# Kernel optimization log

Hardware: AMD Instinct MI355X
Metric: run time of the kernel (lower is better)

The kernel has to match this reference:

```python
import jax, jax.numpy as jnp
import numpy as np

B, D, H, O, E = 8192, 1024, 4096, 1024, 3

def setup_inputs() -> dict:
    key = jax.random.key(0)
    ks = jax.random.split(key, 8)
    s = lambda fan_in: 1.0 / np.sqrt(fan_in)
    return {
        "x":   jax.random.normal(ks[0], (B, D), jnp.float32),
        "gw1": jax.random.normal(ks[1], (D, 256), jnp.float32) * s(D),
        "gb1": jnp.zeros((256,), jnp.float32),
        "gw2": jax.random.normal(ks[2], (256, 128), jnp.float32) * s(256),
        "gb2": jnp.zeros((128,), jnp.float32),
        "gw3": jax.random.normal(ks[3], (128, E), jnp.float32) * s(128),
        "gb3": jnp.zeros((E,), jnp.float32),
        "ew1": jax.random.normal(ks[4], (E, D, H), jnp.float32) * s(D),
        "eb1": jnp.zeros((E, H), jnp.float32),
        "ew2": jax.random.normal(ks[5], (E, H, O), jnp.float32) * s(H),
        "eb2": jnp.zeros((E, O), jnp.float32),
        "top_k": 2,
    }

def reference(x, gw1, gb1, gw2, gb2, gw3, gb3, ew1, eb1, ew2, eb2, top_k):
    # Gating network (dropout is identity in eval mode)
    g = jax.nn.relu(x @ gw1 + gb1)
    g = jax.nn.relu(g @ gw2 + gb2)
    gates = jax.nn.softmax(g @ gw3 + gb3, axis=-1)          # [B, E]

    # top-k routing with renormalized weights
    topk_scores, topk_idx = jax.lax.top_k(gates, top_k)     # [B, k]
    topk_scores = topk_scores / jnp.sum(topk_scores, axis=-1, keepdims=True)

    # scatter normalized scores into dense [B, E] combine weights
    b_ix = jnp.arange(x.shape[0])[:, None]
    combine = jnp.zeros_like(gates).at[b_ix, topk_idx].add(topk_scores)  # [B, E]

    # run all experts densely (small E=3), combine with routing weights
    eh = jax.nn.relu(jnp.einsum('bd,edh->beh', x, ew1) + eb1[None])      # [B, E, H]
    eo = jnp.einsum('beh,eho->beo', eh, ew2) + eb2[None]                 # [B, E, O]
    out = jnp.einsum('be,beo->bo', combine, eo)                          # [B, O]
    return out, gates
```

## Files before the change

### kernel.cpp

```cpp
#include <hip/hip_runtime.h>
#include <cstdint>
#include <cstddef>

#define B_ROWS 8192
#define D_DIM  1024
#define H_DIM  4096
#define O_DIM  1024
#define E_NUM  3
#define K2     (2 * H_DIM)
#define MT_MAX 66
#define SLOT_MAX (MT_MAX * 128)

typedef __attribute__((ext_vector_type(4))) float f4;
typedef __attribute__((ext_vector_type(8))) _Float16 half8;

__device__ __forceinline__ unsigned short f2h_bits(float f) {
  _Float16 h = (_Float16)f;
  return __builtin_bit_cast(unsigned short, h);
}

__device__ __forceinline__ void async16(const void* g, void* l) {
  __builtin_amdgcn_global_load_lds(
      (const __attribute__((address_space(1))) unsigned int*)g,
      (__attribute__((address_space(3))) unsigned int*)l, 16, 0, 0);
}

__global__ __launch_bounds__(256) void k_cast_x(const float* __restrict__ in,
                                                unsigned short* __restrict__ out) {
  size_t i = (size_t)blockIdx.x * 256 + threadIdx.x;
  const f4* p = (const f4*)in;
  f4 a = p[2 * i], b = p[2 * i + 1];
  half8 h;
#pragma unroll
  for (int j = 0; j < 4; ++j) { h[j] = (_Float16)a[j]; h[4 + j] = (_Float16)b[j]; }
  *(half8*)(out + 8 * i) = h;
}

__global__ __launch_bounds__(256) void k_transpose_cast(const float* __restrict__ in,
                                                        unsigned short* __restrict__ out,
                                                        int R, int C) {
  __shared__ float tile[32][33];
  const size_t eoff = (size_t)blockIdx.z * R * C;
  const float* I = in + eoff;
  unsigned short* O = out + eoff;
  int c0 = blockIdx.x * 32, r0 = blockIdx.y * 32;
  int tx = threadIdx.x & 31, ty = threadIdx.x >> 5;
#pragma unroll
  for (int i = 0; i < 4; ++i)
    tile[ty + 8 * i][tx] = I[(size_t)(r0 + ty + 8 * i) * C + c0 + tx];
  __syncthreads();
#pragma unroll
  for (int i = 0; i < 4; ++i)
    O[(size_t)(c0 + ty + 8 * i) * R + r0 + tx] = f2h_bits(tile[tx][ty + 8 * i]);
}

__global__ __launch_bounds__(256) void k_gemm_f32(const float* __restrict__ A,
                                                  const float* __restrict__ Bm,
                                                  const float* __restrict__ bias,
                                                  float* __restrict__ C,
                                                  int N, int K) {
  __shared__ float sAT[16][68];
  __shared__ float sB[16][68];
  const int t = threadIdx.x;
  const int tx = t & 15, ty = t >> 4;
  const int m0 = blockIdx.y * 64, n0 = blockIdx.x * 64;
  float acc[4][4] = {};
  for (int k0 = 0; k0 < K; k0 += 16) {
    __syncthreads();
#pragma unroll
    for (int i = 0; i < 4; ++i) {
      int idx = t + i * 256;
      int r = idx >> 4, c = idx & 15;
      sAT[c][r] = A[(size_t)(m0 + r) * K + (k0 + c)];
      int rb = idx >> 6, cb = idx & 63;
      sB[rb][cb] = Bm[(size_t)(k0 + rb) * N + (n0 + cb)];
    }
    __syncthreads();
#pragma unroll
    for (int kk = 0; kk < 16; ++kk) {
      f4 av = *(const f4*)&sAT[kk][ty * 4];
      f4 bv = *(const f4*)&sB[kk][tx * 4];
#pragma unroll
      for (int i = 0; i < 4; ++i)
#pragma unroll
        for (int j = 0; j < 4; ++j)
          acc[i][j] = fmaf(av[i], bv[j], acc[i][j]);
    }
  }
#pragma unroll
  for (int i = 0; i < 4; ++i) {
    int row = m0 + ty * 4 + i;
    f4 v;
#pragma unroll
    for (int j = 0; j < 4; ++j)
      v[j] = fmaxf(acc[i][j] + bias[n0 + tx * 4 + j], 0.f);
    *(f4*)&C[(size_t)row * N + n0 + tx * 4] = v;
  }
}

__global__ __launch_bounds__(256) void k_gate_topk(const float* __restrict__ h2,
                                                   const float* __restrict__ gw3,
                                                   const float* __restrict__ gb3,
                                                   float* __restrict__ gates,
                                                   float* __restrict__ combine,
                                                   int* __restrict__ bucket) {
  const int lane = threadIdx.x & 63;
  const int row = blockIdx.x * 4 + (threadIdx.x >> 6);
  const float* h = h2 + (size_t)row * 128;
  float h0 = h[lane], h1 = h[lane + 64];
  float l0 = h0 * gw3[lane * 3 + 0] + h1 * gw3[(lane + 64) * 3 + 0];
  float l1 = h0 * gw3[lane * 3 + 1] + h1 * gw3[(lane + 64) * 3 + 1];
  float l2 = h0 * gw3[lane * 3 + 2] + h1 * gw3[(lane + 64) * 3 + 2];
#pragma unroll
  for (int off = 32; off > 0; off >>= 1) {
    l0 += __shfl_down(l0, off);
    l1 += __shfl_down(l1, off);
    l2 += __shfl_down(l2, off);
  }
  if (lane == 0) {
    float g0 = l0 + gb3[0], g1v = l1 + gb3[1], g2v = l2 + gb3[2];
    float mx = fmaxf(g0, fmaxf(g1v, g2v));
    float e0 = expf(g0 - mx), e1 = expf(g1v - mx), e2 = expf(g2v - mx);
    float inv = 1.f / (e0 + e1 + e2);
    float p0 = e0 * inv, p1 = e1 * inv, p2 = e2 * inv;
    gates[row * 3 + 0] = p0; gates[row * 3 + 1] = p1; gates[row * 3 + 2] = p2;
    int amin = 0; float pm = p0;
    if (p1 <= pm) { pm = p1; amin = 1; }
    if (p2 <= pm) { pm = p2; amin = 2; }
    float denom = (p0 + p1 + p2) - pm;
    combine[row * 3 + 0] = (amin == 0) ? 0.f : p0 / denom;
    combine[row * 3 + 1] = (amin == 1) ? 0.f : p1 / denom;
    combine[row * 3 + 2] = (amin == 2) ? 0.f : p2 / denom;
    bucket[row] = amin;
  }
}

__global__ __launch_bounds__(256) void k_count(const int* __restrict__ bucket,
                                               int* __restrict__ cnt) {
  int row = blockIdx.x * 256 + threadIdx.x;
  int b = bucket[row];
  int lane = threadIdx.x & 63;
#pragma unroll
  for (int bid = 0; bid < 3; ++bid) {
    unsigned long long m = __ballot(b == bid);
    if (m && b == bid) {
      int prefix = __popcll(m & ((1ull << lane) - 1));
      if (prefix == 0) atomicAdd(&cnt[bid], __popcll(m));
    }
  }
}

__global__ void k_meta(const int* __restrict__ cnt, int* __restrict__ meta,
                       int* __restrict__ cnt2) {
  int t0 = (cnt[0] + 127) >> 7;
  int t1 = (cnt[1] + 127) >> 7;
  int t2 = (cnt[2] + 127) >> 7;
  meta[0] = 0; meta[1] = t0; meta[2] = t0 + t1; meta[3] = t0 + t1 + t2;
  cnt2[0] = 0; cnt2[1] = 0; cnt2[2] = 0;
}

__global__ __launch_bounds__(256) void k_scatter(const int* __restrict__ bucket,
                                                 const int* __restrict__ meta,
                                                 int* __restrict__ cnt2,
                                                 int* __restrict__ sorted) {
  int row = blockIdx.x * 256 + threadIdx.x;
  int b = bucket[row];
  int lane = threadIdx.x & 63;
#pragma unroll
  for (int bid = 0; bid < 3; ++bid) {
    unsigned long long m = __ballot(b == bid);
    if (m) {
      int cntm = __popcll(m);
      int leader = __ffsll((unsigned long long)m) - 1;
      int base = 0;
      if (lane == leader) base = atomicAdd(&cnt2[bid], cntm);
      base = __shfl(base, leader);
      if (b == bid) {
        int prefix = __popcll(m & ((1ull << lane) - 1));
        sorted[meta[bid] * 128 + base + prefix] = row;
      }
    }
  }
}

__device__ __forceinline__ void bucket_experts(int b, int& ea, int& eb) {
  ea = (b == 0) ? 1 : 0;
  eb = (b == 2) ? 1 : 2;
}

__global__ __launch_bounds__(256) void k_expert_h(const unsigned short* __restrict__ Xh,
                                                  const unsigned short* __restrict__ W1T,
                                                  const float* __restrict__ combine,
                                                  const float* __restrict__ eb1,
                                                  const int* __restrict__ sorted,
                                                  const int* __restrict__ meta,
                                                  unsigned short* __restrict__ EHS) {
  constexpr int K = D_DIM;
  const int mt = blockIdx.x;
  const int tb1 = meta[1], tb2 = meta[2], tb3 = meta[3];
  if (mt >= tb3) return;
  const int b = (mt >= tb2) ? 2 : (mt >= tb1) ? 1 : 0;
  int ea, ebx; bucket_experts(b, ea, ebx);
  const int z = blockIdx.z;
  const int e = z ? ebx : ea;
  const int slot0 = ((b == 0) ? 0 : (b == 1) ? tb1 : tb2) * 128 + (mt - ((b == 0) ? 0 : (b == 1) ? tb1 : tb2)) * 128;
  const int n0 = blockIdx.y * 128;

  __shared__ __align__(16) char smem[32768];
  __shared__ float sC[128];
  char* sA = smem;
  char* sB = smem + 16384;
  const int t = threadIdx.x;
  if (t < 128) {
    int r = sorted[slot0 + t];
    sC[t] = (r < 0) ? 0.f : combine[(size_t)r * 3 + e];
  }

  const unsigned short* aptr[4];
  const unsigned short* bptr[4];
  int soff[4];
#pragma unroll
  for (int i = 0; i < 4; ++i) {
    int sa = t + i * 256;
    int row = sa >> 3;
    int j = (sa & 7) ^ (row & 7);
    soff[i] = sa * 16;
    int r = sorted[slot0 + row];
    int rr = (r < 0) ? 0 : r;
    aptr[i] = Xh + (size_t)rr * K + j * 8;
    bptr[i] = W1T + (size_t)e * H_DIM * K + (size_t)(n0 + row) * K + j * 8;
  }
  const int lane = t & 63;
  const int wm = (t >> 6) & 1, wn = t >> 7;
  const int quad = lane >> 4, l16 = lane & 15;
  int offA[4][2], offB[4][2];
#pragma unroll
  for (int mtile = 0; mtile < 4; ++mtile) {
    int ra = wm * 64 + mtile * 16 + l16;
    int rb = wn * 64 + mtile * 16 + l16;
#pragma unroll
    for (int s = 0; s < 2; ++s) {
      offA[mtile][s] = ra * 128 + (((s * 4 + quad) ^ (ra & 7)) * 16);
      offB[mtile][s] = rb * 128 + (((s * 4 + quad) ^ (rb & 7)) * 16);
    }
  }
  f4 acc[4][4] = {};
  for (int k0 = 0; k0 < K; k0 += 64) {
#pragma unroll
    for (int i = 0; i < 4; ++i) {
      async16(aptr[i] + k0, sA + soff[i]);
      async16(bptr[i] + k0, sB + soff[i]);
    }
    __syncthreads();
#pragma unroll
    for (int s = 0; s < 2; ++s) {
      half8 a[4], bfr[4];
#pragma unroll
      for (int i = 0; i < 4; ++i) a[i] = *(const half8*)(sA + offA[i][s]);
#pragma unroll
      for (int i = 0; i < 4; ++i) bfr[i] = *(const half8*)(sB + offB[i][s]);
#pragma unroll
      for (int i = 0; i < 4; ++i)
#pragma unroll
        for (int jn = 0; jn < 4; ++jn)
          acc[i][jn] = __builtin_amdgcn_mfma_f32_16x16x32_f16(a[i], bfr[jn], acc[i][jn], 0, 0, 0);
    }
    __syncthreads();
  }
  const float* bias = eb1 + (size_t)e * H_DIM;
#pragma unroll
  for (int nt = 0; nt < 4; ++nt) {
    int col = n0 + wn * 64 + nt * 16 + l16;
    float bb = bias[col];
#pragma unroll
    for (int mtile = 0; mtile < 4; ++mtile) {
#pragma unroll
      for (int r = 0; r < 4; ++r) {
        int rloc = wm * 64 + mtile * 16 + quad * 4 + r;
        float v = fmaxf(acc[mtile][nt][r] + bb, 0.f) * sC[rloc];
        EHS[(size_t)(slot0 + rloc) * K2 + (size_t)z * H_DIM + col] = f2h_bits(v);
      }
    }
  }
}

__global__ __launch_bounds__(256) void k_expert_o(const unsigned short* __restrict__ EHS,
                                                  const unsigned short* __restrict__ W2T,
                                                  const float* __restrict__ combine,
                                                  const float* __restrict__ eb2,
                                                  const int* __restrict__ sorted,
                                                  const int* __restrict__ meta,
                                                  float* __restrict__ OUT) {
  const int mt = blockIdx.x;
  const int tb1 = meta[1], tb2 = meta[2], tb3 = meta[3];
  if (mt >= tb3) return;
  const int b = (mt >= tb2) ? 2 : (mt >= tb1) ? 1 : 0;
  int ea, ebx; bucket_experts(b, ea, ebx);
  const int slot0 = mt * 128;
  const int n0 = blockIdx.y * 128;

  __shared__ __align__(16) char smem[32768];
  __shared__ int sRow[128];
  __shared__ float sCa[128], sCb[128];
  char* sA = smem;
  char* sB = smem + 16384;
  const int t = threadIdx.x;
  if (t < 128) {
    int r = sorted[slot0 + t];
    sRow[t] = r;
    int rr = (r < 0) ? 0 : r;
    sCa[t] = combine[(size_t)rr * 3 + ea];
    sCb[t] = combine[(size_t)rr * 3 + ebx];
  }

  const unsigned short* ap[4];
  size_t bpo[4];
  int soff[4];
#pragma unroll
  for (int i = 0; i < 4; ++i) {
    int sa = t + i * 256;
    int row = sa >> 3;
    int j = (sa & 7) ^ (row & 7);
    soff[i] = sa * 16;
    ap[i] = EHS + (size_t)(slot0 + row) * K2 + j * 8;
    bpo[i] = (size_t)(n0 + row) * H_DIM + j * 8;
  }
  const int lane = t & 63;
  const int wm = (t >> 6) & 1, wn = t >> 7;
  const int quad = lane >> 4, l16 = lane & 15;
  int offA[4][2], offB[4][2];
#pragma unroll
  for (int mtile = 0; mtile < 4; ++mtile) {
    int ra = wm * 64 + mtile * 16 + l16;
    int rb = wn * 64 + mtile * 16 + l16;
#pragma unroll
    for (int s = 0; s < 2; ++s) {
      offA[mtile][s] = ra * 128 + (((s * 4 + quad) ^ (ra & 7)) * 16);
      offB[mtile][s] = rb * 128 + (((s * 4 + quad) ^ (rb & 7)) * 16);
    }
  }
  f4 acc[4][4] = {};
#pragma unroll
  for (int half = 0; half < 2; ++half) {
    const int e = half ? ebx : ea;
    const unsigned short* Bb = W2T + (size_t)e * O_DIM * H_DIM;
    const int ka = half * H_DIM;
    for (int k0 = 0; k0 < H_DIM; k0 += 64) {
#pragma unroll
      for (int i = 0; i < 4; ++i) {
        async16(ap[i] + ka + k0, sA + soff[i]);
        async16(Bb + bpo[i] + k0, sB + soff[i]);
      }
      __syncthreads();
#pragma unroll
      for (int s = 0; s < 2; ++s) {
        half8 a[4], bfr[4];
#pragma unroll
        for (int i = 0; i < 4; ++i) a[i] = *(const half8*)(sA + offA[i][s]);
#pragma unroll
        for (int i = 0; i < 4; ++i) bfr[i] = *(const half8*)(sB + offB[i][s]);
#pragma unroll
        for (int i = 0; i < 4; ++i)
#pragma unroll
          for (int jn = 0; jn < 4; ++jn)
            acc[i][jn] = __builtin_amdgcn_mfma_f32_16x16x32_f16(a[i], bfr[jn], acc[i][jn], 0, 0, 0);
      }
      __syncthreads();
    }
  }
#pragma unroll
  for (int nt = 0; nt < 4; ++nt) {
    int col = n0 + wn * 64 + nt * 16 + l16;
    float ba = eb2[(size_t)ea * O_DIM + col];
    float bb = eb2[(size_t)ebx * O_DIM + col];
#pragma unroll
    for (int mtile = 0; mtile < 4; ++mtile) {
#pragma unroll
      for (int r = 0; r < 4; ++r) {
        int rloc = wm * 64 + mtile * 16 + quad * 4 + r;
        int rowg = sRow[rloc];
        if (rowg >= 0) {
          float v = acc[mtile][nt][r] + sCa[rloc] * ba + sCb[rloc] * bb;
          OUT[(size_t)rowg * O_DIM + col] = v;
        }
      }
    }
  }
}

extern "C" void kernel_launch(void* const* d_in, const int* in_sizes, int n_in,
                              void* d_out, int out_size, void* d_ws, size_t ws_size,
                              hipStream_t stream) {
  const float* x   = (const float*)d_in[0];
  const float* gw1 = (const float*)d_in[1];
  const float* gb1 = (const float*)d_in[2];
  const float* gw2 = (const float*)d_in[3];
  const float* gb2 = (const float*)d_in[4];
  const float* gw3 = (const float*)d_in[5];
  const float* gb3 = (const float*)d_in[6];
  const float* ew1 = (const float*)d_in[7];
  const float* eb1 = (const float*)d_in[8];
  const float* ew2 = (const float*)d_in[9];
  const float* eb2 = (const float*)d_in[10];
  float* out = (float*)d_out;
  float* gates = out + (size_t)B_ROWS * O_DIM;

  char* ws = (char*)d_ws;
  size_t off = 0;
  auto take = [&](size_t bytes) -> char* {
    char* p = ws + off;
    off += (bytes + 255) & ~(size_t)255;
    return p;
  };
  unsigned short* xh  = (unsigned short*)take((size_t)B_ROWS * D_DIM * 2);
  unsigned short* w1t = (unsigned short*)take((size_t)E_NUM * H_DIM * D_DIM * 2);
  unsigned short* w2t = (unsigned short*)take((size_t)E_NUM * O_DIM * H_DIM * 2);
  float* comb   = (float*)take((size_t)B_ROWS * 3 * 4);
  float* g1     = (float*)take((size_t)B_ROWS * 256 * 4);
  float* h2     = (float*)take((size_t)B_ROWS * 128 * 4);
  int* bucket   = (int*)take((size_t)B_ROWS * 4);
  int* sorted   = (int*)take((size_t)SLOT_MAX * 4);
  int* cnt      = (int*)take(3 * 4);
  int* cnt2     = (int*)take(3 * 4);
  int* meta     = (int*)take(4 * 4);
  unsigned short* ehs = (unsigned short*)take((size_t)SLOT_MAX * K2 * 2);

  hipMemsetAsync(cnt, 0, 3 * 4, stream);
  hipMemsetAsync(sorted, 0xFF, (size_t)SLOT_MAX * 4, stream);

  k_cast_x<<<dim3(B_ROWS * D_DIM / (256 * 8)), 256, 0, stream>>>(x, xh);
  k_transpose_cast<<<dim3(H_DIM / 32, D_DIM / 32, E_NUM), 256, 0, stream>>>(ew1, w1t, D_DIM, H_DIM);
  k_transpose_cast<<<dim3(O_DIM / 32, H_DIM / 32, E_NUM), 256, 0, stream>>>(ew2, w2t, H_DIM, O_DIM);

  k_gemm_f32<<<dim3(256 / 64, B_ROWS / 64), 256, 0, stream>>>(x, gw1, gb1, g1, 256, D_DIM);
  k_gemm_f32<<<dim3(128 / 64, B_ROWS / 64), 256, 0, stream>>>(g1, gw2, gb2, h2, 128, 256);
  k_gate_topk<<<dim3(B_ROWS / 4), 256, 0, stream>>>(h2, gw3, gb3, gates, comb, bucket);

  k_count<<<dim3(B_ROWS / 256), 256, 0, stream>>>(bucket, cnt);
  k_meta<<<1, 1, 0, stream>>>(cnt, meta, cnt2);
  k_scatter<<<dim3(B_ROWS / 256), 256, 0, stream>>>(bucket, meta, cnt2, sorted);

  k_expert_h<<<dim3(MT_MAX, H_DIM / 128, 2), 256, 0, stream>>>(
      xh, w1t, comb, eb1, sorted, meta, ehs);
  k_expert_o<<<dim3(MT_MAX, O_DIM / 128), 256, 0, stream>>>(
      ehs, w2t, comb, eb2, sorted, meta, out);
}
```

Measured before the change: 812.0 us.

## Split expert output GEMM per expert with atomic accumulation; regroup expert_h block order

The second expert GEMM now launches one block per expert half (z dimension) instead of looping over both experts in one block. This doubles the block count and halves the per-block K loop, and partial results are accumulated into a pre-zeroed output with float atomics. The first GEMM's grid is linearized so that groups of four N-tiles walk all M-tiles together, aimed at better weight reuse in L2. The cost is an extra memset of the output, atomic write traffic, and non-deterministic summation order.

```diff
diff --git a/kernel.cpp b/kernel.cpp
--- a/kernel.cpp
+++ b/kernel.cpp
@@ -196,15 +196,19 @@
                                                   const int* __restrict__ meta,
                                                   unsigned short* __restrict__ EHS) {
   constexpr int K = D_DIM;
-  const int mt = blockIdx.x;
+  const int lin = blockIdx.x;
+  const int group = lin / (MT_MAX * 4);
+  const int rem = lin % (MT_MAX * 4);
+  const int mt = rem % MT_MAX;
+  const int nb = group * 4 + rem / MT_MAX;
   const int tb1 = meta[1], tb2 = meta[2], tb3 = meta[3];
   if (mt >= tb3) return;
   const int b = (mt >= tb2) ? 2 : (mt >= tb1) ? 1 : 0;
   int ea, ebx; bucket_experts(b, ea, ebx);
   const int z = blockIdx.z;
   const int e = z ? ebx : ea;
-  const int slot0 = ((b == 0) ? 0 : (b == 1) ? tb1 : tb2) * 128 + (mt - ((b == 0) ? 0 : (b == 1) ? tb1 : tb2)) * 128;
-  const int n0 = blockIdx.y * 128;
+  const int slot0 = mt * 128;
+  const int n0 = nb * 128;
 
   __shared__ __align__(16) char smem[32768];
   __shared__ float sC[128];
@@ -291,39 +295,41 @@
                                                   const int* __restrict__ sorted,
                                                   const int* __restrict__ meta,
                                                   float* __restrict__ OUT) {
-  const int mt = blockIdx.x;
+  const int mt = blockIdx.y;
   const int tb1 = meta[1], tb2 = meta[2], tb3 = meta[3];
   if (mt >= tb3) return;
   const int b = (mt >= tb2) ? 2 : (mt >= tb1) ? 1 : 0;
   int ea, ebx; bucket_experts(b, ea, ebx);
+  const int z = blockIdx.z;
+  const int e = z ? ebx : ea;
   const int slot0 = mt * 128;
-  const int n0 = blockIdx.y * 128;
+  const int n0 = blockIdx.x * 128;
 
   __shared__ __align__(16) char smem[32768];
   __shared__ int sRow[128];
-  __shared__ float sCa[128], sCb[128];
+  __shared__ float sC[128];
   char* sA = smem;
   char* sB = smem + 16384;
   const int t = threadIdx.x;
   if (t < 128) {
     int r = sorted[slot0 + t];
     sRow[t] = r;
-    int rr = (r < 0) ? 0 : r;
-    sCa[t] = combine[(size_t)rr * 3 + ea];
-    sCb[t] = combine[(size_t)rr * 3 + ebx];
+    sC[t] = (r < 0) ? 0.f : combine[(size_t)r * 3 + e];
   }
 
   const unsigned short* ap[4];
-  size_t bpo[4];
+  const unsigned short* bp[4];
   int soff[4];
+  const unsigned short* Ab = EHS + (size_t)slot0 * K2 + (size_t)z * H_DIM;
+  const unsigned short* Bb = W2T + (size_t)e * O_DIM * H_DIM + (size_t)n0 * H_DIM;
 #pragma unroll
   for (int i = 0; i < 4; ++i) {
     int sa = t + i * 256;
     int row = sa >> 3;
     int j = (sa & 7) ^ (row & 7);
     soff[i] = sa * 16;
-    ap[i] = EHS + (size_t)(slot0 + row) * K2 + j * 8;
-    bpo[i] = (size_t)(n0 + row) * H_DIM + j * 8;
+    ap[i] = Ab + (size_t)row * K2 + j * 8;
+    bp[i] = Bb + (size_t)row * H_DIM + j * 8;
   }
   const int lane = t & 63;
   const int wm = (t >> 6) & 1, wn = t >> 7;
@@ -340,39 +346,32 @@
     }
   }
   f4 acc[4][4] = {};
-#pragma unroll
-  for (int half = 0; half < 2; ++half) {
-    const int e = half ? ebx : ea;
-    const unsigned short* Bb = W2T + (size_t)e * O_DIM * H_DIM;
-    const int ka = half * H_DIM;
-    for (int k0 = 0; k0 < H_DIM; k0 += 64) {
-#pragma unroll
-      for (int i = 0; i < 4; ++i) {
-        async16(ap[i] + ka + k0, sA + soff[i]);
-        async16(Bb + bpo[i] + k0, sB + soff[i]);
-      }
-      __syncthreads();
-#pragma unroll
-      for (int s = 0; s < 2; ++s) {
-        half8 a[4], bfr[4];
-#pragma unroll
-        for (int i = 0; i < 4; ++i) a[i] = *(const half8*)(sA + offA[i][s]);
-#pragma unroll
-        for (int i = 0; i < 4; ++i) bfr[i] = *(const half8*)(sB + offB[i][s]);
-#pragma unroll
-        for (int i = 0; i < 4; ++i)
-#pragma unroll
-          for (int jn = 0; jn < 4; ++jn)
-            acc[i][jn] = __builtin_amdgcn_mfma_f32_16x16x32_f16(a[i], bfr[jn], acc[i][jn], 0, 0, 0);
-      }
-      __syncthreads();
-    }
+  for (int k0 = 0; k0 < H_DIM; k0 += 64) {
+#pragma unroll
+    for (int i = 0; i < 4; ++i) {
+      async16(ap[i] + k0, sA + soff[i]);
+      async16(bp[i] + k0, sB + soff[i]);
+    }
+    __syncthreads();
+#pragma unroll
+    for (int s = 0; s < 2; ++s) {
+      half8 a[4], bfr[4];
+#pragma unroll
+      for (int i = 0; i < 4; ++i) a[i] = *(const half8*)(sA + offA[i][s]);
+#pragma unroll
+      for (int i = 0; i < 4; ++i) bfr[i] = *(const half8*)(sB + offB[i][s]);
+#pragma unroll
+      for (int i = 0; i < 4; ++i)
+#pragma unroll
+        for (int jn = 0; jn < 4; ++jn)
+          acc[i][jn] = __builtin_amdgcn_mfma_f32_16x16x32_f16(a[i], bfr[jn], acc[i][jn], 0, 0, 0);
+    }
+    __syncthreads();
   }
 #pragma unroll
   for (int nt = 0; nt < 4; ++nt) {
     int col = n0 + wn * 64 + nt * 16 + l16;
-    float ba = eb2[(size_t)ea * O_DIM + col];
-    float bb = eb2[(size_t)ebx * O_DIM + col];
+    float be = eb2[(size_t)e * O_DIM + col];
 #pragma unroll
     for (int mtile = 0; mtile < 4; ++mtile) {
 #pragma unroll
@@ -380,8 +379,8 @@
         int rloc = wm * 64 + mtile * 16 + quad * 4 + r;
         int rowg = sRow[rloc];
         if (rowg >= 0) {
-          float v = acc[mtile][nt][r] + sCa[rloc] * ba + sCb[rloc] * bb;
-          OUT[(size_t)rowg * O_DIM + col] = v;
+          float v = acc[mtile][nt][r] + sC[rloc] * be;
+          atomicAdd(&OUT[(size_t)rowg * O_DIM + col], v);
         }
       }
     }
@@ -427,6 +426,7 @@
 
   hipMemsetAsync(cnt, 0, 3 * 4, stream);
   hipMemsetAsync(sorted, 0xFF, (size_t)SLOT_MAX * 4, stream);
+  hipMemsetAsync(out, 0, (size_t)B_ROWS * O_DIM * 4, stream);
 
   k_cast_x<<<dim3(B_ROWS * D_DIM / (256 * 8)), 256, 0, stream>>>(x, xh);
   k_transpose_cast<<<dim3(H_DIM / 32, D_DIM / 32, E_NUM), 256, 0, stream>>>(ew1, w1t, D_DIM, H_DIM);
@@ -440,8 +440,8 @@
   k_meta<<<1, 1, 0, stream>>>(cnt, meta, cnt2);
   k_scatter<<<dim3(B_ROWS / 256), 256, 0, stream>>>(bucket, meta, cnt2, sorted);
 
-  k_expert_h<<<dim3(MT_MAX, H_DIM / 128, 2), 256, 0, stream>>>(
+  k_expert_h<<<dim3(MT_MAX * 32, 1, 2), 256, 0, stream>>>(
       xh, w1t, comb, eb1, sorted, meta, ehs);
-  k_expert_o<<<dim3(MT_MAX, O_DIM / 128), 256, 0, stream>>>(
+  k_expert_o<<<dim3(O_DIM / 128, MT_MAX, 2), 256, 0, stream>>>(
       ehs, w2t, comb, eb2, sorted, meta, out);
 }
```

Result: slower. 853.8 us (+5.1%).
